# Optimization experiments

Measured on AMD Instinct MI355X. Metric: run time of the kernel, lower is better.

Reference implementation:

```python
import jax, jax.numpy as jnp
import numpy as np

VOCAB = 50000
EMB = 200        # embedding_size
CAP = 3          # capitalization_size
IN = EMB + CAP   # LSTM input size = 203
HID = 128        # LSTMCell(128)
B = 256
T = 500          # comment_length
NC = 6           # num_classes
DENSE = 64


def _lstm_scan(x_tbi, W, b):
    """x_tbi: [T,B,IN]. W: [IN+HID, 4*HID] (tf gate order i, j, f, o), b: [4*HID].
    Returns h sequence [T,B,HID]. forget_bias=1.0 as in tf.contrib.rnn.LSTMCell."""
    h0 = jnp.zeros((x_tbi.shape[1], HID), x_tbi.dtype)

    def step(carry, x):
        h, c = carry
        gates = jnp.concatenate([x, h], axis=-1) @ W + b   # [B, 4*HID]
        i, j, f, o = jnp.split(gates, 4, axis=-1)
        c = jax.nn.sigmoid(f + 1.0) * c + jax.nn.sigmoid(i) * jnp.tanh(j)
        h = jax.nn.sigmoid(o) * jnp.tanh(c)
        return (h, c), h

    _, hs = jax.lax.scan(step, (h0, h0), x_tbi)
    return hs


def setup_inputs() -> dict:
    key = jax.random.key(0)
    ks = jax.random.split(key, 12)
    words = jax.random.randint(ks[0], (B, T), 0, VOCAB, dtype=jnp.int32)
    capitals = jax.random.randint(ks[1], (B, T), 0, CAP, dtype=jnp.int32)
    # word embeddings: random trainable table with a trailing zero-padding row
    word_emb = jax.random.normal(ks[2], (VOCAB + 1, EMB), dtype=jnp.float32) * 0.1
    # capitalization embedding: one_hot_embedding_matrix(3) = [eye(3); zeros(1,3)]
    cap_emb = jnp.concatenate([jnp.eye(CAP, dtype=jnp.float32),
                               jnp.zeros((1, CAP), dtype=jnp.float32)], axis=0)
    def glorot(k, shape):
        lim = np.sqrt(6.0 / (shape[0] + shape[1]))
        return jax.random.uniform(k, shape, jnp.float32, -lim, lim)
    W_fw = glorot(ks[3], (IN + HID, 4 * HID))
    b_fw = jnp.zeros((4 * HID,), jnp.float32)
    W_bw = glorot(ks[4], (IN + HID, 4 * HID))
    b_bw = jnp.zeros((4 * HID,), jnp.float32)
    W1 = glorot(ks[5], (2 * HID, DENSE))
    b1 = jnp.zeros((DENSE,), jnp.float32)
    W2 = glorot(ks[6], (DENSE, NC))
    b2 = jnp.zeros((NC,), jnp.float32)
    return {"words": words, "capitals": capitals, "word_emb": word_emb,
            "cap_emb": cap_emb, "W_fw": W_fw, "b_fw": b_fw,
            "W_bw": W_bw, "b_bw": b_bw, "W1": W1, "b1": b1,
            "W2": W2, "b2": b2}


def reference(words, capitals, word_emb, cap_emb, W_fw, b_fw, W_bw, b_bw,
              W1, b1, W2, b2):
    # embedding lookups and concat -> [B, T, 203]
    x = jnp.concatenate([word_emb[words], cap_emb[capitals]], axis=-1)
    x_tbi = jnp.transpose(x, (1, 0, 2))                    # [T, B, IN]
    # forward direction: take output at last timestep
    h_fw_last = _lstm_scan(x_tbi, W_fw, b_fw)[-1]          # [B, HID]
    # backward direction: bidirectional_dynamic_rnn reverses bw outputs back,
    # so outputs[1][:, 0, :] == last state of scan over the reversed sequence
    h_bw_first = _lstm_scan(x_tbi[::-1], W_bw, b_bw)[-1]   # [B, HID]
    rnn_output = jnp.concatenate([h_fw_last, h_bw_first], axis=1)  # [B, 256]
    dense1 = jax.nn.elu(rnn_output @ W1 + b1)              # [B, 64]
    y_hat = jax.nn.sigmoid(dense1 @ W2 + b2)               # [B, NC]
    return y_hat
```

## Files before the change

kernel.cpp:

```cpp
#include <hip/hip_runtime.h>

#define T 500
#define NB 256
#define VROWS 50001
#define EMB 200
#define KPAD 224
#define LOG2E 1.44269504f

typedef unsigned short u16;
typedef __attribute__((ext_vector_type(8))) __bf16 bf16x8;
typedef __attribute__((ext_vector_type(8))) short short8;
typedef __attribute__((ext_vector_type(8))) u16 u16x8;
typedef __attribute__((ext_vector_type(4))) float f32x4;
typedef __attribute__((ext_vector_type(4))) u16 u16x4;

__device__ __forceinline__ u16 f2bf(float x) {
  __bf16 h = (__bf16)x;
  return __builtin_bit_cast(u16, h);
}
__device__ __forceinline__ float bf2f(u16 b) {
  union { unsigned u; float f; } v; v.u = ((unsigned)b) << 16;
  return v.f;
}
__device__ __forceinline__ float rcp_(float x) { return __builtin_amdgcn_rcpf(x); }
__device__ __forceinline__ float ex2_(float x) { return __builtin_amdgcn_exp2f(x); }
__device__ __forceinline__ float gsc(int g) { return (g == 1) ? 2.f * LOG2E : -LOG2E; }

__global__ void prep_kernel(const float* __restrict__ cap_emb,
                            const float* __restrict__ Wfw, const float* __restrict__ bfw,
                            const float* __restrict__ Wbw, const float* __restrict__ bbw,
                            float* __restrict__ Cproj, u16* __restrict__ Bt) {
  const int S2 = 2 * 512 * KPAD;
  const int S3 = 2 * 4 * 512;
  int tid = blockIdx.x * blockDim.x + threadIdx.x;
  int nthr = gridDim.x * blockDim.x;
  for (int i = tid; i < S2 + S3; i += nthr) {
    if (i < S2) {
      int d = i / (512 * KPAD), rem = i - d * (512 * KPAD);
      int colp = rem / KPAD, k = rem - colp * KPAD;
      const float* W = d ? Wbw : Wfw;
      int g = colp & 3, jj = colp >> 2;
      Bt[i] = (k < EMB) ? f2bf(W[k * 512 + g * 128 + jj] * gsc(g)) : (u16)0;
    } else {
      int idx = i - S2;
      int dir = idx >> 11; int c = (idx >> 9) & 3; int colp = idx & 511;
      int j = colp >> 2, g = colp & 3;
      const float* W = dir ? Wbw : Wfw;
      const float* bias = dir ? bbw : bfw;
      float v = bias[g * 128 + j] + (g == 2 ? 1.f : 0.f);
      #pragma unroll
      for (int cc = 0; cc < 3; ++cc)
        v += cap_emb[c * 3 + cc] * W[(200 + cc) * 512 + g * 128 + j];
      Cproj[idx] = v * gsc(g);
    }
  }
}

__global__ __launch_bounds__(256) void xproj_kernel(
    const int* __restrict__ words, const int* __restrict__ caps,
    const float* __restrict__ word_emb, const u16* __restrict__ Bt,
    const float* __restrict__ Cproj, u16* __restrict__ XP) {
  const int mt = blockIdx.x, nt = blockIdx.y, dir = blockIdx.z;
  const u16* __restrict__ B = Bt + (size_t)dir * 512 * KPAD;
  const float* __restrict__ Cb = Cproj + dir * 4 * 512;
  u16* __restrict__ xp = XP + (size_t)dir * T * NB * 512;

  __shared__ u16 As[2][128 * 32];
  __shared__ u16 Bs[2][128 * 32];

  const int tid = threadIdx.x;
  const int w = tid >> 6, l = tid & 63;
  const int la = l & 15, lb = l >> 4;
  const int m0 = mt * 128, n0 = nt * 128;
  const int tblk = m0 >> 8;

  const int ar = tid >> 1, ah = tid & 1;
  const int ab = (m0 & 255) + ar;
  const int aword = words[ab * T + tblk];
  const float* __restrict__ aemb = word_emb + (size_t)aword * EMB;

  auto stageA = [&](int buf, int ks) {
    int kbase = ks * 32 + ah * 16;
    u16x8 lo, hi;
    #pragma unroll
    for (int q = 0; q < 4; ++q) {
      int k = kbase + q * 4;
      f32x4 v;
      if (k < EMB) v = *(const f32x4*)(aemb + k);
      else v = f32x4{0.f, 0.f, 0.f, 0.f};
      u16 b0 = f2bf(v[0]), b1 = f2bf(v[1]), b2 = f2bf(v[2]), b3 = f2bf(v[3]);
      if (q < 2) { lo[q*4+0]=b0; lo[q*4+1]=b1; lo[q*4+2]=b2; lo[q*4+3]=b3; }
      else { int qq=q-2; hi[qq*4+0]=b0; hi[qq*4+1]=b1; hi[qq*4+2]=b2; hi[qq*4+3]=b3; }
    }
    *(u16x8*)&As[buf][ar * 32 + ah * 16]     = lo;
    *(u16x8*)&As[buf][ar * 32 + ah * 16 + 8] = hi;
  };
  auto stageB = [&](int buf, int ks) {
    int k0 = ks * 32;
    #pragma unroll
    for (int h = 0; h < 2; ++h) {
      int c = w * 128 + h * 64 + l;
      int row = c >> 2, kq = c & 3;
      const u16* gb = B + (size_t)(n0 + row) * KPAD + k0 + kq * 8;
      __builtin_amdgcn_global_load_lds(
          (const __attribute__((address_space(1))) void*)gb,
          (__attribute__((address_space(3))) void*)&Bs[buf][(w * 128 + h * 64) * 8],
          16, 0, 0);
    }
  };

  f32x4 z = {0.f, 0.f, 0.f, 0.f};
  f32x4 acc[4][4] = {{z,z,z,z},{z,z,z,z},{z,z,z,z},{z,z,z,z}};
  const int wr = w >> 1, wc = w & 1;

  stageA(0, 0); stageB(0, 0);
  __syncthreads();
  #pragma unroll 1
  for (int ks = 0; ks < 7; ++ks) {
    int cur = ks & 1;
    if (ks < 6) { stageA(cur ^ 1, ks + 1); stageB(cur ^ 1, ks + 1); }
    bf16x8 af[4], bfr[4];
    #pragma unroll
    for (int m = 0; m < 4; ++m)
      af[m] = *(const bf16x8*)&As[cur][(wr * 64 + m * 16 + la) * 32 + lb * 8];
    #pragma unroll
    for (int n = 0; n < 4; ++n)
      bfr[n] = *(const bf16x8*)&Bs[cur][(wc * 64 + n * 16 + la) * 32 + lb * 8];
    #pragma unroll
    for (int m = 0; m < 4; ++m)
      #pragma unroll
      for (int n = 0; n < 4; ++n)
        acc[m][n] = __builtin_amdgcn_mfma_f32_16x16x32_bf16(af[m], bfr[n], acc[m][n], 0, 0, 0);
    __syncthreads();
  }

  #pragma unroll
  for (int m = 0; m < 4; ++m) {
    #pragma unroll
    for (int r = 0; r < 4; ++r) {
      int b = (m0 & 255) + wr * 64 + m * 16 + lb * 4 + r;
      int cap = caps[b * T + tblk];
      const float* cbr = Cb + cap * 512;
      u16* op = xp + ((size_t)tblk * NB + b) * 512;
      #pragma unroll
      for (int n = 0; n < 4; ++n) {
        int colp = n0 + wc * 64 + n * 16 + la;
        op[colp] = f2bf(acc[m][n][r] + cbr[colp]);
      }
    }
  }
}

template <int PAR>
__device__ __forceinline__ void lstm_step(
    int t, int dir, int la, int lb, int j,
    const u16* __restrict__ xpd, int voff0, int voff1, int voff2, int voff3,
    const bf16x8 (&bfrag)[4][4], u16* __restrict__ hbuf,
    u16x4 (&xc)[4],
    u16x4 (&xg)[4],
    f32x4& cst, f32x4& hl) {
  const u16* hb = hbuf + PAR * 2048;
  const int swz = (la & 7) << 3;
  bf16x8 afr[4];
  #pragma unroll
  for (int kk = 0; kk < 4; ++kk)
    afr[kk] = *(const bf16x8*)(hb + ((la * 128 + kk * 32 + lb * 8) ^ swz));

  {
    int ts = t + 2; if (ts > T - 1) ts = T - 1;
    int tt = dir ? (T - 1 - ts) : ts;
    const u16* p = xpd + (size_t)tt * (NB * 512);
    xg[0] = *(const u16x4*)(p + voff0);
    xg[1] = *(const u16x4*)(p + voff1);
    xg[2] = *(const u16x4*)(p + voff2);
    xg[3] = *(const u16x4*)(p + voff3);
  }

  f32x4 acc0, acc1, acc2, acc3;
  #pragma unroll
  for (int r = 0; r < 4; ++r) {
    acc0[r] = bf2f(xc[r][0]);
    acc1[r] = bf2f(xc[r][1]);
    acc2[r] = bf2f(xc[r][2]);
    acc3[r] = bf2f(xc[r][3]);
  }
  __builtin_amdgcn_s_setprio(1);
  #pragma unroll
  for (int kk = 0; kk < 4; ++kk) {
    acc0 = __builtin_amdgcn_mfma_f32_16x16x32_bf16(afr[kk], bfrag[0][kk], acc0, 0, 0, 0);
    acc1 = __builtin_amdgcn_mfma_f32_16x16x32_bf16(afr[kk], bfrag[1][kk], acc1, 0, 0, 0);
    acc2 = __builtin_amdgcn_mfma_f32_16x16x32_bf16(afr[kk], bfrag[2][kk], acc2, 0, 0, 0);
    acc3 = __builtin_amdgcn_mfma_f32_16x16x32_bf16(afr[kk], bfrag[3][kk], acc3, 0, 0, 0);
  }
  __builtin_amdgcn_s_setprio(0);
  u16* ho = hbuf + (PAR ^ 1) * 2048;
  #pragma unroll
  for (int r = 0; r < 4; ++r) {
    float ig = rcp_(1.f + ex2_(acc0[r]));
    float tj = 1.f - 2.f * rcp_(1.f + ex2_(acc1[r]));
    float fg = rcp_(1.f + ex2_(acc2[r]));
    float cn = fg * cst[r] + ig * tj;
    cst[r] = cn;
    float og = rcp_(1.f + ex2_(acc3[r]));
    float hn = og * (1.f - 2.f * rcp_(1.f + ex2_(2.f * LOG2E * cn)));
    hl[r] = hn;
    int row = lb * 4 + r;
    ho[(row * 128 + j) ^ ((row & 7) << 3)] = f2bf(hn);
  }
  __builtin_amdgcn_sched_barrier(0);
  asm volatile("s_waitcnt lgkmcnt(0)");
  __builtin_amdgcn_s_barrier();
  __builtin_amdgcn_sched_barrier(0);
}

__global__ __launch_bounds__(512, 1) void lstm_kernel(
    const u16* __restrict__ XP, const float* __restrict__ Wfw,
    const float* __restrict__ Wbw, float* __restrict__ rnn) {
  const int dir = blockIdx.x & 1;
  const int chunk = blockIdx.x >> 1;
  const int b0 = chunk * 16;
  const u16* __restrict__ xpd = XP + (size_t)dir * T * NB * 512;
  const float* __restrict__ W = dir ? Wbw : Wfw;

  const int tid = threadIdx.x;
  const int w = tid >> 6, l = tid & 63, la = l & 15, lb = l >> 4;
  const int j = w * 16 + la;

  const int voff0 = (b0 + lb * 4 + 0) * 512 + j * 4;
  const int voff1 = (b0 + lb * 4 + 1) * 512 + j * 4;
  const int voff2 = (b0 + lb * 4 + 2) * 512 + j * 4;
  const int voff3 = (b0 + lb * 4 + 3) * 512 + j * 4;

  bf16x8 bfrag[4][4];
  #pragma unroll
  for (int g = 0; g < 4; ++g) {
    #pragma unroll
    for (int kk = 0; kk < 4; ++kk) {
      short8 t8;
      #pragma unroll
      for (int r = 0; r < 8; ++r) {
        int k = kk * 32 + lb * 8 + r;
        t8[r] = (short)f2bf(W[(203 + k) * 512 + g * 128 + j] * gsc(g));
      }
      bfrag[g][kk] = __builtin_bit_cast(bf16x8, t8);
    }
  }

  __shared__ u16 hbuf[2 * 16 * 128];
  for (int i = tid; i < 2 * 16 * 128; i += 512) hbuf[i] = 0;

  f32x4 cst = {0.f, 0.f, 0.f, 0.f};
  f32x4 hl  = {0.f, 0.f, 0.f, 0.f};

  u16x4 xA[4], xB[4], xC[4], xD[4];
  {
    int tt0 = dir ? (T - 1) : 0;
    int tt1 = dir ? (T - 2) : 1;
    const u16* p0 = xpd + (size_t)tt0 * (NB * 512);
    const u16* p1 = xpd + (size_t)tt1 * (NB * 512);
    xA[0] = *(const u16x4*)(p0 + voff0); xA[1] = *(const u16x4*)(p0 + voff1);
    xA[2] = *(const u16x4*)(p0 + voff2); xA[3] = *(const u16x4*)(p0 + voff3);
    xB[0] = *(const u16x4*)(p1 + voff0); xB[1] = *(const u16x4*)(p1 + voff1);
    xB[2] = *(const u16x4*)(p1 + voff2); xB[3] = *(const u16x4*)(p1 + voff3);
  }
  __syncthreads();

  #pragma unroll 1
  for (int tq = 0; tq < T / 4; ++tq) {
    int t0 = 4 * tq;
    lstm_step<0>(t0,     dir, la, lb, j, xpd, voff0, voff1, voff2, voff3,
                 bfrag, hbuf, xA, xC, cst, hl);
    lstm_step<1>(t0 + 1, dir, la, lb, j, xpd, voff0, voff1, voff2, voff3,
                 bfrag, hbuf, xB, xD, cst, hl);
    lstm_step<0>(t0 + 2, dir, la, lb, j, xpd, voff0, voff1, voff2, voff3,
                 bfrag, hbuf, xC, xA, cst, hl);
    lstm_step<1>(t0 + 3, dir, la, lb, j, xpd, voff0, voff1, voff2, voff3,
                 bfrag, hbuf, xD, xB, cst, hl);
  }

  #pragma unroll
  for (int r = 0; r < 4; ++r)
    rnn[(size_t)(b0 + lb * 4 + r) * 256 + dir * 128 + j] = hl[r];
}

__global__ void head_kernel(const float* __restrict__ rnn, const float* __restrict__ W1,
                            const float* __restrict__ b1, const float* __restrict__ W2,
                            const float* __restrict__ b2, float* __restrict__ out) {
  int b = blockIdx.x;
  int jj = threadIdx.x;
  __shared__ float d1[64];
  float acc = b1[jj];
  const float* r = rnn + b * 256;
  #pragma unroll 4
  for (int k = 0; k < 256; ++k) acc += r[k] * W1[k * 64 + jj];
  d1[jj] = acc > 0.f ? acc : (__expf(acc) - 1.f);
  __syncthreads();
  if (jj < 6) {
    float a2 = b2[jj];
    #pragma unroll 8
    for (int k = 0; k < 64; ++k) a2 += d1[k] * W2[k * 6 + jj];
    out[b * 6 + jj] = rcp_(1.f + __expf(-a2));
  }
}

extern "C" void kernel_launch(void* const* d_in, const int* in_sizes, int n_in,
                              void* d_out, int out_size, void* d_ws, size_t ws_size,
                              hipStream_t stream) {
  (void)in_sizes; (void)n_in; (void)out_size; (void)ws_size;
  const int*   words    = (const int*)  d_in[0];
  const int*   caps     = (const int*)  d_in[1];
  const float* word_emb = (const float*)d_in[2];
  const float* cap_emb  = (const float*)d_in[3];
  const float* Wfw      = (const float*)d_in[4];
  const float* bfw      = (const float*)d_in[5];
  const float* Wbw      = (const float*)d_in[6];
  const float* bbw      = (const float*)d_in[7];
  const float* W1       = (const float*)d_in[8];
  const float* b1       = (const float*)d_in[9];
  const float* W2       = (const float*)d_in[10];
  const float* b2       = (const float*)d_in[11];
  float* out = (float*)d_out;

  char* base = (char*)d_ws;
  size_t off = 0;
  auto alloc = [&](size_t bytes) {
    char* q = base + off;
    off = (off + bytes + 255) & ~(size_t)255;
    return q;
  };
  u16*   XP     = (u16*)  alloc((size_t)2 * T * NB * 512 * 2);
  u16*   Bt     = (u16*)  alloc((size_t)2 * 512 * KPAD * 2);
  float* Cproj  = (float*)alloc((size_t)2 * 4 * 512 * 4);
  float* rnn    = (float*)alloc((size_t)256 * 256 * 4);

  hipLaunchKernelGGL(prep_kernel, dim3(256), dim3(256), 0, stream,
                     cap_emb, Wfw, bfw, Wbw, bbw, Cproj, Bt);
  hipLaunchKernelGGL(xproj_kernel, dim3(1000, 4, 2), dim3(256), 0, stream,
                     words, caps, word_emb, Bt, Cproj, XP);
  hipLaunchKernelGGL(lstm_kernel, dim3(32), dim3(512), 0, stream,
                     XP, Wfw, Wbw, rnn);
  hipLaunchKernelGGL(head_kernel, dim3(256), dim3(64), 0, stream,
                     rnn, W1, b1, W2, b2, out);
}
```

Before: 700.7 us.

## Swizzle xproj LDS tiles, stage epilogue through LDS, and fuse LSTM gate reciprocals

The input-projection GEMM now XOR-swizzles its A and B shared-memory tiles to avoid bank conflicts. It splits the A-tile prefetch into an early global load and a late LDS write so the load overlaps the MFMAs. Its epilogue goes through a shared-memory transpose so each thread writes contiguous 16-byte bf16 vectors instead of scattered 2-byte stores. The LSTM cell math merges the sigmoid and tanh reciprocals into fewer rcp calls, shortening the serial per-step critical path. The merged products of exponentials could overflow for large gate preactivations, which changes numerical edge behaviour.

```diff
diff --git a/kernel.cpp b/kernel.cpp
--- a/kernel.cpp
+++ b/kernel.cpp
@@ -13,6 +13,9 @@
 typedef __attribute__((ext_vector_type(8))) u16 u16x8;
 typedef __attribute__((ext_vector_type(4))) float f32x4;
 typedef __attribute__((ext_vector_type(4))) u16 u16x4;
+
+#define AS1 __attribute__((address_space(1)))
+#define AS3 __attribute__((address_space(3)))
 
 __device__ __forceinline__ u16 f2bf(float x) {
   __bf16 h = (__bf16)x;
@@ -62,92 +65,118 @@
     const float* __restrict__ Cproj, u16* __restrict__ XP) {
   const int mt = blockIdx.x, nt = blockIdx.y, dir = blockIdx.z;
   const u16* __restrict__ B = Bt + (size_t)dir * 512 * KPAD;
-  const float* __restrict__ Cb = Cproj + dir * 4 * 512;
   u16* __restrict__ xp = XP + (size_t)dir * T * NB * 512;
 
-  __shared__ u16 As[2][128 * 32];
-  __shared__ u16 Bs[2][128 * 32];
+  __shared__ __align__(16) char pool[34048];
+  u16* As = (u16*)pool;
+  u16* Bs = (u16*)(pool + 16384);
+  float (*Cls)[132] = (float(*)[132])pool;
 
   const int tid = threadIdx.x;
   const int w = tid >> 6, l = tid & 63;
   const int la = l & 15, lb = l >> 4;
-  const int m0 = mt * 128, n0 = nt * 128;
-  const int tblk = m0 >> 8;
-
-  const int ar = tid >> 1, ah = tid & 1;
-  const int ab = (m0 & 255) + ar;
-  const int aword = words[ab * T + tblk];
-  const float* __restrict__ aemb = word_emb + (size_t)aword * EMB;
-
-  auto stageA = [&](int buf, int ks) {
-    int kbase = ks * 32 + ah * 16;
+  const int wr = w >> 1, wc = w & 1;
+  const int tblk = mt >> 1;
+  const int bbase = (mt & 1) * 128;
+  const int n0 = nt * 128;
+
+  const int arow = tid >> 1, khalf = tid & 1;
+  const int wd = words[(bbase + arow) * T + tblk];
+  const float* __restrict__ aemb = word_emb + (size_t)wd * EMB;
+  const int aswz0 = (arow * 4 + ((khalf * 2 + 0) ^ (arow & 3))) * 8;
+  const int aswz1 = (arow * 4 + ((khalf * 2 + 1) ^ (arow & 3))) * 8;
+
+  const int s0 = w * 128 + l, s1 = w * 128 + 64 + l;
+  const int brn0 = s0 >> 2, bc0 = (s0 & 3) ^ (brn0 & 3);
+  const int brn1 = s1 >> 2, bc1 = (s1 & 3) ^ (brn1 & 3);
+  const u16* bsrc0 = B + (size_t)(n0 + brn0) * KPAD + bc0 * 8;
+  const u16* bsrc1 = B + (size_t)(n0 + brn1) * KPAD + bc1 * 8;
+
+  f32x4 va[4];
+  auto loadA = [&](int ks) {
+    #pragma unroll
+    for (int q = 0; q < 4; ++q)
+      va[q] = *(const f32x4*)(aemb + ks * 32 + khalf * 16 + q * 4);
+  };
+  auto writeA = [&](int buf) {
     u16x8 lo, hi;
     #pragma unroll
-    for (int q = 0; q < 4; ++q) {
-      int k = kbase + q * 4;
-      f32x4 v;
-      if (k < EMB) v = *(const f32x4*)(aemb + k);
-      else v = f32x4{0.f, 0.f, 0.f, 0.f};
-      u16 b0 = f2bf(v[0]), b1 = f2bf(v[1]), b2 = f2bf(v[2]), b3 = f2bf(v[3]);
-      if (q < 2) { lo[q*4+0]=b0; lo[q*4+1]=b1; lo[q*4+2]=b2; lo[q*4+3]=b3; }
-      else { int qq=q-2; hi[qq*4+0]=b0; hi[qq*4+1]=b1; hi[qq*4+2]=b2; hi[qq*4+3]=b3; }
-    }
-    *(u16x8*)&As[buf][ar * 32 + ah * 16]     = lo;
-    *(u16x8*)&As[buf][ar * 32 + ah * 16 + 8] = hi;
+    for (int e = 0; e < 4; ++e) {
+      lo[e] = f2bf(va[0][e]); lo[4 + e] = f2bf(va[1][e]);
+      hi[e] = f2bf(va[2][e]); hi[4 + e] = f2bf(va[3][e]);
+    }
+    *(u16x8*)&As[buf * 4096 + aswz0] = lo;
+    *(u16x8*)&As[buf * 4096 + aswz1] = hi;
   };
   auto stageB = [&](int buf, int ks) {
-    int k0 = ks * 32;
-    #pragma unroll
-    for (int h = 0; h < 2; ++h) {
-      int c = w * 128 + h * 64 + l;
-      int row = c >> 2, kq = c & 3;
-      const u16* gb = B + (size_t)(n0 + row) * KPAD + k0 + kq * 8;
-      __builtin_amdgcn_global_load_lds(
-          (const __attribute__((address_space(1))) void*)gb,
-          (__attribute__((address_space(3))) void*)&Bs[buf][(w * 128 + h * 64) * 8],
-          16, 0, 0);
-    }
+    __builtin_amdgcn_global_load_lds(
+        (const AS1 void*)(bsrc0 + ks * 32),
+        (AS3 void*)&Bs[buf * 4096 + (w * 128) * 8], 16, 0, 0);
+    __builtin_amdgcn_global_load_lds(
+        (const AS1 void*)(bsrc1 + ks * 32),
+        (AS3 void*)&Bs[buf * 4096 + (w * 128 + 64) * 8], 16, 0, 0);
   };
 
   f32x4 z = {0.f, 0.f, 0.f, 0.f};
   f32x4 acc[4][4] = {{z,z,z,z},{z,z,z,z},{z,z,z,z},{z,z,z,z}};
-  const int wr = w >> 1, wc = w & 1;
-
-  stageA(0, 0); stageB(0, 0);
+
+  loadA(0);
+  stageB(0, 0);
+  writeA(0);
   __syncthreads();
+
   #pragma unroll 1
   for (int ks = 0; ks < 7; ++ks) {
-    int cur = ks & 1;
-    if (ks < 6) { stageA(cur ^ 1, ks + 1); stageB(cur ^ 1, ks + 1); }
+    const int cur = ks & 1;
+    if (ks < 6) { stageB(cur ^ 1, ks + 1); loadA(ks + 1); }
     bf16x8 af[4], bfr[4];
     #pragma unroll
-    for (int m = 0; m < 4; ++m)
-      af[m] = *(const bf16x8*)&As[cur][(wr * 64 + m * 16 + la) * 32 + lb * 8];
-    #pragma unroll
-    for (int n = 0; n < 4; ++n)
-      bfr[n] = *(const bf16x8*)&Bs[cur][(wc * 64 + n * 16 + la) * 32 + lb * 8];
+    for (int m = 0; m < 4; ++m) {
+      int ra = wr * 64 + m * 16 + la;
+      af[m] = *(const bf16x8*)&As[cur * 4096 + ra * 32 + ((lb ^ (ra & 3)) * 8)];
+    }
+    #pragma unroll
+    for (int n = 0; n < 4; ++n) {
+      int rn = wc * 64 + n * 16 + la;
+      bfr[n] = *(const bf16x8*)&Bs[cur * 4096 + rn * 32 + ((lb ^ (rn & 3)) * 8)];
+    }
     #pragma unroll
     for (int m = 0; m < 4; ++m)
       #pragma unroll
       for (int n = 0; n < 4; ++n)
         acc[m][n] = __builtin_amdgcn_mfma_f32_16x16x32_bf16(af[m], bfr[n], acc[m][n], 0, 0, 0);
+    if (ks < 6) writeA(cur ^ 1);
     __syncthreads();
   }
 
-  #pragma unroll
-  for (int m = 0; m < 4; ++m) {
-    #pragma unroll
-    for (int r = 0; r < 4; ++r) {
-      int b = (m0 & 255) + wr * 64 + m * 16 + lb * 4 + r;
-      int cap = caps[b * T + tblk];
-      const float* cbr = Cb + cap * 512;
-      u16* op = xp + ((size_t)tblk * NB + b) * 512;
-      #pragma unroll
-      for (int n = 0; n < 4; ++n) {
-        int colp = n0 + wc * 64 + n * 16 + la;
-        op[colp] = f2bf(acc[m][n][r] + cbr[colp]);
+  const int rrow = tid >> 1, rch = tid & 1;
+  const int rb = bbase + rrow;
+  const int rcap = caps[rb * T + tblk];
+  const float* __restrict__ cbase = Cproj + (dir * 4 + rcap) * 512;
+  u16* __restrict__ rop = xp + ((size_t)tblk * NB + rb) * 512;
+
+  #pragma unroll
+  for (int pass = 0; pass < 2; ++pass) {
+    if (wc == pass) {
+      #pragma unroll
+      for (int m = 0; m < 4; ++m)
+        #pragma unroll
+        for (int n = 0; n < 4; ++n)
+          *(f32x4*)&Cls[n * 16 + la][wr * 64 + m * 16 + lb * 4] = acc[m][n];
+    }
+    __syncthreads();
+    int colp0 = n0 + pass * 64 + rch * 32;
+    #pragma unroll
+    for (int s = 0; s < 4; ++s) {
+      u16x8 o;
+      #pragma unroll
+      for (int e = 0; e < 8; ++e) {
+        int cl = rch * 32 + s * 8 + e;
+        o[e] = f2bf(Cls[cl][rrow] + cbase[colp0 + s * 8 + e]);
       }
-    }
+      *(u16x8*)(rop + colp0 + s * 8) = o;
+    }
+    __syncthreads();
   }
 }
 
@@ -196,13 +225,15 @@
   u16* ho = hbuf + (PAR ^ 1) * 2048;
   #pragma unroll
   for (int r = 0; r < 4; ++r) {
-    float ig = rcp_(1.f + ex2_(acc0[r]));
-    float tj = 1.f - 2.f * rcp_(1.f + ex2_(acc1[r]));
-    float fg = rcp_(1.f + ex2_(acc2[r]));
-    float cn = fg * cst[r] + ig * tj;
+    float ei = ex2_(acc0[r]);
+    float ej = ex2_(acc1[r]);
+    float ef = ex2_(acc2[r]);
+    float eo = ex2_(acc3[r]);
+    float itj = (ej - 1.f) * rcp_((1.f + ei) * (1.f + ej));
+    float cn = cst[r] * rcp_(1.f + ef) + itj;
     cst[r] = cn;
-    float og = rcp_(1.f + ex2_(acc3[r]));
-    float hn = og * (1.f - 2.f * rcp_(1.f + ex2_(2.f * LOG2E * cn)));
+    float E = ex2_(2.f * LOG2E * cn);
+    float hn = (E - 1.f) * rcp_((1.f + eo) * (1.f + E));
     hl[r] = hn;
     int row = lb * 4 + r;
     ho[(row * 128 + j) ^ ((row & 7) << 3)] = f2bf(hn);
```

New measurement: 668.5 us. -4.6%, faster.
